# Optimization experiments

Hardware: AMD Instinct MI355X
Metric: run time of the kernel (lower is better)

The kernel has to match this reference:

```python
import jax, jax.numpy as jnp
import numpy as np

N, E, G = 50000, 400000, 64
F_IN, HID, HEADS, GF, NCLS = 16, 128, 4, 10, 6


def _init(k, shape, fan):
    return jax.random.normal(k, shape, jnp.float32) * (1.0 / np.sqrt(fan))


def setup_inputs() -> dict:
    key = jax.random.key(0)
    ks = jax.random.split(key, 16)
    x = jax.random.normal(ks[0], (N, F_IN), jnp.float32)
    edge_index = jax.random.randint(ks[1], (2, E), 0, N)
    batch = jnp.sort(jax.random.randint(ks[2], (N,), 0, G))
    graph_feat = jax.random.normal(ks[3], (G, GF), jnp.float32)
    # GATConv 1: in=16 -> heads=4, out=128, concat
    W1 = _init(ks[4], (F_IN, HEADS * HID), F_IN)
    att_src1 = _init(ks[5], (HEADS, HID), HID)
    att_dst1 = _init(ks[6], (HEADS, HID), HID)
    b1 = jnp.zeros((HEADS * HID,), jnp.float32)
    # GATConv 2: in=512 -> heads=1, out=128, mean (concat=False)
    W2 = _init(ks[7], (HEADS * HID, HID), HEADS * HID)
    att_src2 = _init(ks[8], (1, HID), HID)
    att_dst2 = _init(ks[9], (1, HID), HID)
    b2 = jnp.zeros((HID,), jnp.float32)
    # graph_proj MLP 10->32->32
    Wg1 = _init(ks[10], (GF, 32), GF); bg1 = jnp.zeros((32,), jnp.float32)
    Wg2 = _init(ks[11], (32, 32), 32); bg2 = jnp.zeros((32,), jnp.float32)
    # classifier 160->128->6
    Wc1 = _init(ks[12], (HID + 32, 128), HID + 32); bc1 = jnp.zeros((128,), jnp.float32)
    Wc2 = _init(ks[13], (128, NCLS), 128); bc2 = jnp.zeros((NCLS,), jnp.float32)
    return dict(x=x, edge_index=edge_index, batch=batch, graph_feat=graph_feat,
                W1=W1, att_src1=att_src1, att_dst1=att_dst1, b1=b1,
                W2=W2, att_src2=att_src2, att_dst2=att_dst2, b2=b2,
                Wg1=Wg1, bg1=bg1, Wg2=Wg2, bg2=bg2,
                Wc1=Wc1, bc1=bc1, Wc2=Wc2, bc2=bc2)


def gat_layer(x, W, att_src, att_dst, bias, src, dst, n_nodes, heads, out_dim, concat):
    # Linear transform: [N, H, C]
    h = (x @ W).reshape(n_nodes, heads, out_dim)
    a_src = jnp.einsum('nhc,hc->nh', h, att_src)  # [N,H]
    a_dst = jnp.einsum('nhc,hc->nh', h, att_dst)  # [N,H]
    e = jax.nn.leaky_relu(a_src[src] + a_dst[dst], 0.2)  # [Etot,H]
    # segment softmax over edges grouped by dst (self-loops ensure nonempty)
    m = jax.ops.segment_max(e, dst, num_segments=n_nodes)
    ex = jnp.exp(e - m[dst])
    denom = jax.ops.segment_sum(ex, dst, num_segments=n_nodes)
    alpha = ex / denom[dst]  # [Etot,H]
    out = jax.ops.segment_sum(alpha[:, :, None] * h[src], dst, num_segments=n_nodes)  # [N,H,C]
    if concat:
        out = out.reshape(n_nodes, heads * out_dim)
    else:
        out = out.mean(axis=1)
    return out + bias


def reference(x, edge_index, batch, graph_feat,
              W1, att_src1, att_dst1, b1,
              W2, att_src2, att_dst2, b2,
              Wg1, bg1, Wg2, bg2, Wc1, bc1, Wc2, bc2):
    n = x.shape[0]
    loops = jnp.arange(n, dtype=edge_index.dtype)
    src = jnp.concatenate([edge_index[0], loops])
    dst = jnp.concatenate([edge_index[1], loops])
    h = jax.nn.elu(gat_layer(x, W1, att_src1, att_dst1, b1, src, dst, n, HEADS, HID, True))
    h = jax.nn.elu(gat_layer(h, W2, att_src2, att_dst2, b2, src, dst, n, 1, HID, False))
    # global mean pool over graphs
    g = graph_feat.shape[0]
    sums = jax.ops.segment_sum(h, batch, num_segments=g)
    counts = jax.ops.segment_sum(jnp.ones((n, 1), h.dtype), batch, num_segments=g)
    pooled = sums / jnp.maximum(counts, 1.0)
    gf = jax.nn.relu(graph_feat @ Wg1 + bg1) @ Wg2 + bg2
    z = jnp.concatenate([pooled, gf], axis=1)
    z = jax.nn.relu(z @ Wc1 + bc1)
    return z @ Wc2 + bc2
```

## Files before the change

### kernel.cpp

```cpp
#include <hip/hip_runtime.h>
#include <hip/hip_bf16.h>

#define NN 50000
#define EE 400000
#define GG 64
#define CAP 48
#define HROW 520

typedef unsigned short u16;
typedef unsigned char u8;
typedef long long i64;
typedef unsigned long long u64;
typedef __attribute__((ext_vector_type(8))) short bf16x8;
typedef __attribute__((ext_vector_type(4))) float f32x4;
typedef __attribute__((ext_vector_type(2))) float f32x2;

__device__ __forceinline__ float b2f(u16 u) {
    unsigned int x = ((unsigned int)u) << 16;
    return __uint_as_float(x);
}
__device__ __forceinline__ u16 f2b(float f) {
    unsigned int x = __float_as_uint(f);
    unsigned int r = x + 0x7fffu + ((x >> 16) & 1u);
    return (u16)(r >> 16);
}
__device__ __forceinline__ u8 f2fp8(float f) {
    return (u8)(__builtin_amdgcn_cvt_pk_fp8_f32(f, f, 0, false) & 0xFF);
}
__device__ __forceinline__ f32x2 fp8x2_f32(unsigned int v, bool hi) {
    return hi ? __builtin_amdgcn_cvt_pk_f32_fp8(v, true)
              : __builtin_amdgcn_cvt_pk_f32_fp8(v, false);
}
__device__ __forceinline__ float wred_sum(float v) {
    #pragma unroll
    for (int o = 32; o; o >>= 1) v += __shfl_xor(v, o, 64);
    return v;
}
__device__ __forceinline__ float lrelu(float v) { return v > 0.f ? v : 0.2f * v; }

__global__ void k_prep(const int* __restrict__ batch, int* __restrict__ deg,
                       int* __restrict__ col, int* __restrict__ gstart,
                       const float* __restrict__ W1, const float* __restrict__ as1,
                       const float* __restrict__ ad1, u16* __restrict__ W1p,
                       const float* __restrict__ W2, u8* __restrict__ W2p,
                       float* __restrict__ pooled) {
    __shared__ float asw[16][8];
    int b = blockIdx.x, t = threadIdx.x;
    if (b < 196) {
        int n = b * 256 + t;
        if (n < NN) { deg[n] = 1; col[(size_t)n * CAP] = n; }
    } else if (b == 196) {
        if (t <= GG) {
            int lo = 0, hi = NN;
            while (lo < hi) {
                int mid = (lo + hi) >> 1;
                if (batch[mid] < t) lo = mid + 1; else hi = mid;
            }
            gstart[t] = lo;
        }
    } else if (b < 453) {
        int idx = (b - 197) * 256 + t;
        int j = idx & 7;
        int l = (idx >> 3) & 63;
        int ct = idx >> 9;
        int c = ct >> 3, tt = ct & 7;
        int p = c * 32 + (l >> 4) * 8 + j;
        int lp = p >> 3, jp = p & 7;
        int chan = 128 * (lp >> 4) + 16 * jp + (lp & 15);
        int n = tt * 16 + (l & 15);
        W2p[idx] = f2fp8(W2[chan * 128 + n]);
    } else if (b == 453) {
        int pair = t >> 1, half = t & 1;
        int k = pair >> 3, h = pair & 7;
        int hd = h & 3;
        const float* att = (h >= 4) ? ad1 : as1;
        float s = 0.f;
        int c0 = half * 64;
        for (int c = c0; c < c0 + 64; c++)
            s += W1[k * 512 + hd * 128 + c] * att[hd * 128 + c];
        s += __shfl_xor(s, 1, 64);
        if (half == 0) asw[k][h] = s;
        __syncthreads();
        for (int idx = t; idx < 33 * 64 * 8; idx += 256) {
            int j = idx & 7, l = (idx >> 3) & 63, tt = idx >> 9;
            int quad = l >> 4, m = l & 15;
            int k2 = quad * 8 + j;
            float v = 0.f;
            if (k2 < 16) {
                if (tt < 32) v = W1[k2 * 512 + tt * 16 + m];
                else if (m < 8) v = asw[k2][m];
            }
            W1p[idx] = f2b(v);
        }
    } else {
        for (int i = t; i < GG * 128; i += 256) pooled[i] = 0.f;
    }
}

__global__ void k_edges(const int* __restrict__ ei, int* __restrict__ deg,
                        int* __restrict__ col) {
    int e = blockIdx.x * 256 + threadIdx.x;
    if (e < EE) {
        int s = ei[e];
        int d = ei[EE + e];
        int slot = atomicAdd(&deg[d], 1);
        if (slot < CAP) col[(size_t)d * CAP + slot] = s;
    }
}

__global__ __launch_bounds__(256) void k_gemm1(
    const float* __restrict__ x, const u16* __restrict__ W1p,
    u8* __restrict__ h1, float* __restrict__ a_src1, float* __restrict__ a_dst1) {
    int tid = threadIdx.x;
    int wave = tid >> 6, l = tid & 63;
    int quad = l >> 4, m = l & 15;
    int row0 = blockIdx.x * 64 + wave * 16;
    int arow = row0 + m;
    int arow_c = arow < NN ? arow : (NN - 1);
    bf16x8 af;
    if (quad < 2) {
        const float* xp = x + arow_c * 16 + quad * 8;
        float4 x0 = *(const float4*)(xp);
        float4 x1 = *(const float4*)(xp + 4);
        u16 tmp[8] = {f2b(x0.x), f2b(x0.y), f2b(x0.z), f2b(x0.w),
                      f2b(x1.x), f2b(x1.y), f2b(x1.z), f2b(x1.w)};
        af = *(bf16x8*)tmp;
    } else {
        af = (bf16x8){0, 0, 0, 0, 0, 0, 0, 0};
    }
    const u16* bp = W1p + l * 8;
    f32x4 acc[33];
    #pragma unroll
    for (int tt = 0; tt < 33; tt++) acc[tt] = (f32x4){0.f, 0.f, 0.f, 0.f};
    #pragma unroll
    for (int tt = 0; tt < 33; tt++) {
        bf16x8 bf = *(const bf16x8*)(bp + (size_t)tt * 512);
        acc[tt] = __builtin_amdgcn_mfma_f32_16x16x32_bf16(af, bf, acc[tt], 0, 0, 0);
    }
    #pragma unroll
    for (int r = 0; r < 4; r++) {
        int row = row0 + quad * 4 + r;
        if (row >= NN) continue;
        unsigned int d[8];
        #pragma unroll
        for (int dd = 0; dd < 8; dd++) {
            unsigned int w = __builtin_amdgcn_cvt_pk_fp8_f32(acc[4 * dd][r], acc[4 * dd + 1][r], 0, false);
            w = __builtin_amdgcn_cvt_pk_fp8_f32(acc[4 * dd + 2][r], acc[4 * dd + 3][r], w, true);
            d[dd] = w;
        }
        uint4 v0; v0.x = d[0]; v0.y = d[1]; v0.z = d[2]; v0.w = d[3];
        uint4 v1; v1.x = d[4]; v1.y = d[5]; v1.z = d[6]; v1.w = d[7];
        *(uint4*)(h1 + (size_t)row * 512 + m * 32) = v0;
        *(uint4*)(h1 + (size_t)row * 512 + m * 32 + 16) = v1;
        float v = acc[32][r];
        if (m < 4) a_src1[row * 4 + m] = v;
        else if (m < 8) a_dst1[row * 4 + (m - 4)] = v;
    }
}

__global__ __launch_bounds__(256) void k_mid(
    const int* __restrict__ deg, const int* __restrict__ col,
    const float* __restrict__ a_src1, const float* __restrict__ a_dst1,
    const u8* __restrict__ h1, const float* __restrict__ b1,
    const u8* __restrict__ W2p, const float* __restrict__ as2,
    const float* __restrict__ ad2, u8* __restrict__ hL2,
    float* __restrict__ a_src2, float* __restrict__ a_dst2) {
    __shared__ u64 hrowq[16 * HROW / 8];
    __shared__ float alphaS[4][64][4];
    __shared__ float part[16][2][4];
    u8* hrow = (u8*)hrowq;
    int t = threadIdx.x;
    int w = t >> 6, l = t & 63;
    int n0 = blockIdx.x * 16;
    int g = l >> 4, m = l & 15;
    const u8* hb = h1 + m * 32 + g * 8;
    for (int i = 0; i < 4; i++) {
        int n = n0 + w * 4 + i;
        int dg = min(deg[n], CAP);
        int sl = (l < dg) ? col[(size_t)n * CAP + l] : 0;
        float4 ad = *(const float4*)(a_dst1 + n * 4);
        float4 as = *(const float4*)(a_src1 + (size_t)sl * 4);
        float4 e;
        e.x = __expf(lrelu(as.x + ad.x)); e.y = __expf(lrelu(as.y + ad.y));
        e.z = __expf(lrelu(as.z + ad.z)); e.w = __expf(lrelu(as.w + ad.w));
        if (l >= dg) e = (float4){0.f, 0.f, 0.f, 0.f};
        float4 inv;
        inv.x = 1.0f / wred_sum(e.x);
        inv.y = 1.0f / wred_sum(e.y);
        inv.z = 1.0f / wred_sum(e.z);
        inv.w = 1.0f / wred_sum(e.w);
        {
            float4 a4;
            a4.x = e.x * inv.x; a4.y = e.y * inv.y;
            a4.z = e.z * inv.z; a4.w = e.w * inv.w;
            *(float4*)&alphaS[w][l][0] = a4;
        }
        f32x2 acc[4] = {{0.f, 0.f}, {0.f, 0.f}, {0.f, 0.f}, {0.f, 0.f}};
        int iters = (dg + 3) >> 2;
        for (int j = 0; j < iters; j++) {
            int e0 = 4 * j, e1 = 4 * j + 1, e2 = 4 * j + 2, e3 = 4 * j + 3;
            int s0 = __shfl(sl, e0), s1 = __shfl(sl, e1);
            int s2 = __shfl(sl, e2), s3 = __shfl(sl, e3);
            float a0 = alphaS[w][e0][g], a1 = alphaS[w][e1][g];
            float a2 = alphaS[w][e2][g], a3 = alphaS[w][e3][g];
            uint2 u0 = *(const uint2*)(hb + (size_t)s0 * 512);
            uint2 u1 = *(const uint2*)(hb + (size_t)s1 * 512);
            uint2 u2 = *(const uint2*)(hb + (size_t)s2 * 512);
            uint2 u3 = *(const uint2*)(hb + (size_t)s3 * 512);
            acc[0] += a0 * fp8x2_f32(u0.x, false);
            acc[1] += a0 * fp8x2_f32(u0.x, true);
            acc[2] += a0 * fp8x2_f32(u0.y, false);
            acc[3] += a0 * fp8x2_f32(u0.y, true);
            acc[0] += a1 * fp8x2_f32(u1.x, false);
            acc[1] += a1 * fp8x2_f32(u1.x, true);
            acc[2] += a1 * fp8x2_f32(u1.y, false);
            acc[3] += a1 * fp8x2_f32(u1.y, true);
            acc[0] += a2 * fp8x2_f32(u2.x, false);
            acc[1] += a2 * fp8x2_f32(u2.x, true);
            acc[2] += a2 * fp8x2_f32(u2.y, false);
            acc[3] += a2 * fp8x2_f32(u2.y, true);
            acc[0] += a3 * fp8x2_f32(u3.x, false);
            acc[1] += a3 * fp8x2_f32(u3.x, true);
            acc[2] += a3 * fp8x2_f32(u3.y, false);
            acc[3] += a3 * fp8x2_f32(u3.y, true);
        }
        float av[8] = {acc[0].x, acc[0].y, acc[1].x, acc[1].y,
                       acc[2].x, acc[2].y, acc[3].x, acc[3].y};
        const float* bb = b1 + 128 * g + m;
        float v[8];
        #pragma unroll
        for (int j = 0; j < 8; j++) {
            float q = av[j] + bb[16 * j];
            v[j] = q > 0.f ? q : __expf(q) - 1.0f;
        }
        unsigned int d0 = __builtin_amdgcn_cvt_pk_fp8_f32(v[0], v[1], 0, false);
        d0 = __builtin_amdgcn_cvt_pk_fp8_f32(v[2], v[3], d0, true);
        unsigned int d1 = __builtin_amdgcn_cvt_pk_fp8_f32(v[4], v[5], 0, false);
        d1 = __builtin_amdgcn_cvt_pk_fp8_f32(v[6], v[7], d1, true);
        uint2 ov; ov.x = d0; ov.y = d1;
        *(uint2*)(hrow + (w * 4 + i) * HROW + l * 8) = ov;
    }
    __syncthreads();
    int quad = l >> 4;
    int tt0 = 2 * w;
    const u8* bbase = W2p + l * 8;
    f32x4 accA = (f32x4){0.f, 0.f, 0.f, 0.f};
    f32x4 accB = (f32x4){0.f, 0.f, 0.f, 0.f};
    #pragma unroll
    for (int c = 0; c < 16; c++) {
        i64 af = *(const i64*)(hrow + m * HROW + c * 32 + quad * 8);
        i64 bf0 = *(const i64*)(bbase + (size_t)(c * 8 + tt0) * 512);
        i64 bf1 = *(const i64*)(bbase + (size_t)(c * 8 + tt0 + 1) * 512);
        accA = __builtin_amdgcn_mfma_f32_16x16x32_fp8_fp8(af, bf0, accA, 0, 0, 0);
        accB = __builtin_amdgcn_mfma_f32_16x16x32_fp8_fp8(af, bf1, accB, 0, 0, 0);
    }
    float as0 = as2[tt0 * 16 + m], ad0 = ad2[tt0 * 16 + m];
    float as1v = as2[(tt0 + 1) * 16 + m], ad1v = ad2[(tt0 + 1) * 16 + m];
    #pragma unroll
    for (int r = 0; r < 4; r++) {
        int node = n0 + quad * 4 + r;
        float v0 = accA[r], v1 = accB[r];
        hL2[(size_t)node * 128 + tt0 * 16 + m] = f2fp8(v0);
        hL2[(size_t)node * 128 + (tt0 + 1) * 16 + m] = f2fp8(v1);
        float rs = v0 * as0 + v1 * as1v;
        float rd = v0 * ad0 + v1 * ad1v;
        #pragma unroll
        for (int o = 1; o < 16; o <<= 1) {
            rs += __shfl_xor(rs, o, 64);
            rd += __shfl_xor(rd, o, 64);
        }
        if (m == 0) { part[quad * 4 + r][0][w] = rs; part[quad * 4 + r][1][w] = rd; }
    }
    __syncthreads();
    if (t < 32) {
        int row = t >> 1, which = t & 1;
        float s = part[row][which][0] + part[row][which][1] +
                  part[row][which][2] + part[row][which][3];
        if (which) a_dst2[n0 + row] = s; else a_src2[n0 + row] = s;
    }
}

__global__ __launch_bounds__(256) void k_agg2(
    const int* __restrict__ deg, const int* __restrict__ col,
    const float* __restrict__ a_src2, const float* __restrict__ a_dst2,
    const u8* __restrict__ hL2, const float* __restrict__ b2v,
    const int* __restrict__ batch, float* __restrict__ pooled) {
    __shared__ float red[4][128];
    __shared__ int gS[4];
    int t = threadIdx.x;
    int wave = t >> 6, l = t & 63;
    int n = blockIdx.x * 4 + wave;
    if (n >= NN) return;
    int dg = min(deg[n], CAP);
    int sl = (l < dg) ? col[(size_t)n * CAP + l] : 0;
    float ad = a_dst2[n];
    float e = (l < dg) ? __expf(lrelu(a_src2[sl] + ad)) : 0.f;
    float inv = 1.0f / wred_sum(e);
    float al = e * inv;
    f32x2 acc = {0.f, 0.f};
    const u8* hb = hL2 + l * 2;
    int iters = (dg + 3) >> 2;
    for (int j = 0; j < iters; j++) {
        int e0 = 4 * j, e1 = 4 * j + 1, e2 = 4 * j + 2, e3 = 4 * j + 3;
        int s0 = __shfl(sl, e0), s1 = __shfl(sl, e1);
        int s2 = __shfl(sl, e2), s3 = __shfl(sl, e3);
        float a0 = __shfl(al, e0), a1 = __shfl(al, e1);
        float a2 = __shfl(al, e2), a3 = __shfl(al, e3);
        unsigned int u0 = *(const u16*)(hb + (size_t)s0 * 128);
        unsigned int u1 = *(const u16*)(hb + (size_t)s1 * 128);
        unsigned int u2 = *(const u16*)(hb + (size_t)s2 * 128);
        unsigned int u3 = *(const u16*)(hb + (size_t)s3 * 128);
        acc += a0 * fp8x2_f32(u0, false);
        acc += a1 * fp8x2_f32(u1, false);
        acc += a2 * fp8x2_f32(u2, false);
        acc += a3 * fp8x2_f32(u3, false);
    }
    float o0 = acc.x + b2v[2 * l];     o0 = o0 > 0.f ? o0 : __expf(o0) - 1.0f;
    float o1 = acc.y + b2v[2 * l + 1]; o1 = o1 > 0.f ? o1 : __expf(o1) - 1.0f;
    red[wave][2 * l] = o0;
    red[wave][2 * l + 1] = o1;
    if (l == 0) gS[wave] = batch[n];
    __syncthreads();
    if (t < 128) {
        int g0 = gS[0];
        if (gS[1] == g0 && gS[2] == g0 && gS[3] == g0) {
            float s = red[0][t] + red[1][t] + red[2][t] + red[3][t];
            atomicAdd(&pooled[g0 * 128 + t], s);
        } else {
            #pragma unroll
            for (int w = 0; w < 4; w++)
                atomicAdd(&pooled[gS[w] * 128 + t], red[w][t]);
        }
    }
}

__global__ __launch_bounds__(128) void k_head(
    const int* __restrict__ gstart, const float* __restrict__ pooled,
    const float* __restrict__ gfeat,
    const float* __restrict__ Wg1, const float* __restrict__ bg1,
    const float* __restrict__ Wg2, const float* __restrict__ bg2,
    const float* __restrict__ Wc1, const float* __restrict__ bc1,
    const float* __restrict__ Wc2, const float* __restrict__ bc2,
    float* __restrict__ out) {
    __shared__ float z[160];
    __shared__ float hg[32];
    __shared__ float c1b[128];
    int g = blockIdx.x, t = threadIdx.x;
    float cntf = (float)(gstart[g + 1] - gstart[g]);
    z[t] = pooled[g * 128 + t] / fmaxf(cntf, 1.0f);
    if (t < 32) {
        float a = bg1[t];
        for (int i = 0; i < 10; i++) a += gfeat[g * 10 + i] * Wg1[i * 32 + t];
        hg[t] = fmaxf(a, 0.f);
    }
    __syncthreads();
    if (t < 32) {
        float a = bg2[t];
        for (int i = 0; i < 32; i++) a += hg[i] * Wg2[i * 32 + t];
        z[128 + t] = a;
    }
    __syncthreads();
    float a = bc1[t];
    for (int i = 0; i < 160; i++) a += z[i] * Wc1[i * 128 + t];
    c1b[t] = fmaxf(a, 0.f);
    __syncthreads();
    if (t < 6) {
        float o = bc2[t];
        for (int i = 0; i < 128; i++) o += c1b[i] * Wc2[i * 6 + t];
        out[g * 6 + t] = o;
    }
}

extern "C" void kernel_launch(void* const* d_in, const int* in_sizes, int n_in,
                              void* d_out, int out_size, void* d_ws, size_t ws_size,
                              hipStream_t stream) {
    const float* x     = (const float*)d_in[0];
    const int*   ei    = (const int*)d_in[1];
    const int*   batch = (const int*)d_in[2];
    const float* gfeat = (const float*)d_in[3];
    const float* W1    = (const float*)d_in[4];
    const float* as1   = (const float*)d_in[5];
    const float* ad1   = (const float*)d_in[6];
    const float* b1    = (const float*)d_in[7];
    const float* W2    = (const float*)d_in[8];
    const float* as2   = (const float*)d_in[9];
    const float* ad2   = (const float*)d_in[10];
    const float* b2    = (const float*)d_in[11];
    const float* Wg1   = (const float*)d_in[12];
    const float* bg1   = (const float*)d_in[13];
    const float* Wg2   = (const float*)d_in[14];
    const float* bg2   = (const float*)d_in[15];
    const float* Wc1   = (const float*)d_in[16];
    const float* bc1   = (const float*)d_in[17];
    const float* Wc2   = (const float*)d_in[18];
    const float* bc2   = (const float*)d_in[19];
    float* out = (float*)d_out;

    size_t off = 0;
    char* base = (char*)d_ws;
    auto take = [&](size_t nbytes) -> char* {
        char* p = base + off;
        off = (off + nbytes + 255) & ~(size_t)255;
        return p;
    };
    u8*    h1     = (u8*)take((size_t)NN * 512);
    u8*    hL2    = (u8*)take((size_t)NN * 128);
    float* a_src1 = (float*)take((size_t)NN * 4 * 4);
    float* a_dst1 = (float*)take((size_t)NN * 4 * 4);
    float* a_src2 = (float*)take((size_t)NN * 4);
    float* a_dst2 = (float*)take((size_t)NN * 4);
    int*   deg    = (int*)take((size_t)NN * 4);
    int*   col    = (int*)take((size_t)NN * CAP * 4);
    float* pooled = (float*)take(GG * 128 * 4);
    int*   gstart = (int*)take((GG + 1) * 4);
    u8*    W2p    = (u8*)take((size_t)512 * 128);
    u16*   W1p    = (u16*)take((size_t)33 * 64 * 8 * 2);
    (void)ws_size; (void)in_sizes; (void)n_in; (void)out_size;

    k_prep<<<455, 256, 0, stream>>>(batch, deg, col, gstart, W1, as1, ad1, W1p,
                                    W2, W2p, pooled);
    k_edges<<<(EE + 255) / 256, 256, 0, stream>>>(ei, deg, col);
    k_gemm1<<<(NN + 63) / 64, 256, 0, stream>>>(x, W1p, h1, a_src1, a_dst1);
    k_mid<<<NN / 16, 256, 0, stream>>>(deg, col, a_src1, a_dst1, h1, b1,
                                       W2p, as2, ad2, hL2, a_src2, a_dst2);
    k_agg2<<<(NN + 3) / 4, 256, 0, stream>>>(deg, col, a_src2, a_dst2, hL2, b2,
                                             batch, pooled);
    k_head<<<GG, 128, 0, stream>>>(gstart, pooled, gfeat, Wg1, bg1, Wg2, bg2,
                                   Wc1, bc1, Wc2, bc2, out);
}
```

Measured before the change: 243.9 us.

## Assign one wave per node in k_mid with 1024-thread blocks

```diff
diff --git a/kernel.cpp b/kernel.cpp
--- a/kernel.cpp
+++ b/kernel.cpp
@@ -158,7 +158,7 @@
     }
 }
 
-__global__ __launch_bounds__(256) void k_mid(
+__global__ __launch_bounds__(1024) void k_mid(
     const int* __restrict__ deg, const int* __restrict__ col,
     const float* __restrict__ a_src1, const float* __restrict__ a_dst1,
     const u8* __restrict__ h1, const float* __restrict__ b1,
@@ -166,16 +166,15 @@
     const float* __restrict__ ad2, u8* __restrict__ hL2,
     float* __restrict__ a_src2, float* __restrict__ a_dst2) {
     __shared__ u64 hrowq[16 * HROW / 8];
-    __shared__ float alphaS[4][64][4];
-    __shared__ float part[16][2][4];
+    __shared__ float alphaS[16][64][4];
+    __shared__ float part[16][2][8];
     u8* hrow = (u8*)hrowq;
     int t = threadIdx.x;
     int w = t >> 6, l = t & 63;
     int n0 = blockIdx.x * 16;
     int g = l >> 4, m = l & 15;
-    const u8* hb = h1 + m * 32 + g * 8;
-    for (int i = 0; i < 4; i++) {
-        int n = n0 + w * 4 + i;
+    {
+        int n = n0 + w;
         int dg = min(deg[n], CAP);
         int sl = (l < dg) ? col[(size_t)n * CAP + l] : 0;
         float4 ad = *(const float4*)(a_dst1 + n * 4);
@@ -195,34 +194,28 @@
             a4.z = e.z * inv.z; a4.w = e.w * inv.w;
             *(float4*)&alphaS[w][l][0] = a4;
         }
+        const u8* hb = h1 + m * 32 + g * 8;
         f32x2 acc[4] = {{0.f, 0.f}, {0.f, 0.f}, {0.f, 0.f}, {0.f, 0.f}};
-        int iters = (dg + 3) >> 2;
+        int iters = (dg + 7) >> 3;
         for (int j = 0; j < iters; j++) {
-            int e0 = 4 * j, e1 = 4 * j + 1, e2 = 4 * j + 2, e3 = 4 * j + 3;
-            int s0 = __shfl(sl, e0), s1 = __shfl(sl, e1);
-            int s2 = __shfl(sl, e2), s3 = __shfl(sl, e3);
-            float a0 = alphaS[w][e0][g], a1 = alphaS[w][e1][g];
-            float a2 = alphaS[w][e2][g], a3 = alphaS[w][e3][g];
-            uint2 u0 = *(const uint2*)(hb + (size_t)s0 * 512);
-            uint2 u1 = *(const uint2*)(hb + (size_t)s1 * 512);
-            uint2 u2 = *(const uint2*)(hb + (size_t)s2 * 512);
-            uint2 u3 = *(const uint2*)(hb + (size_t)s3 * 512);
-            acc[0] += a0 * fp8x2_f32(u0.x, false);
-            acc[1] += a0 * fp8x2_f32(u0.x, true);
-            acc[2] += a0 * fp8x2_f32(u0.y, false);
-            acc[3] += a0 * fp8x2_f32(u0.y, true);
-            acc[0] += a1 * fp8x2_f32(u1.x, false);
-            acc[1] += a1 * fp8x2_f32(u1.x, true);
-            acc[2] += a1 * fp8x2_f32(u1.y, false);
-            acc[3] += a1 * fp8x2_f32(u1.y, true);
-            acc[0] += a2 * fp8x2_f32(u2.x, false);
-            acc[1] += a2 * fp8x2_f32(u2.x, true);
-            acc[2] += a2 * fp8x2_f32(u2.y, false);
-            acc[3] += a2 * fp8x2_f32(u2.y, true);
-            acc[0] += a3 * fp8x2_f32(u3.x, false);
-            acc[1] += a3 * fp8x2_f32(u3.x, true);
-            acc[2] += a3 * fp8x2_f32(u3.y, false);
-            acc[3] += a3 * fp8x2_f32(u3.y, true);
+            #pragma unroll
+            for (int q = 0; q < 8; q += 2) {
+                int eA = 8 * j + q, eB = 8 * j + q + 1;
+                int sA = __shfl(sl, eA);
+                int sB = __shfl(sl, eB);
+                float aA = alphaS[w][eA][g];
+                float aB = alphaS[w][eB][g];
+                uint2 uA = *(const uint2*)(hb + (size_t)sA * 512);
+                uint2 uB = *(const uint2*)(hb + (size_t)sB * 512);
+                acc[0] += aA * fp8x2_f32(uA.x, false);
+                acc[1] += aA * fp8x2_f32(uA.x, true);
+                acc[2] += aA * fp8x2_f32(uA.y, false);
+                acc[3] += aA * fp8x2_f32(uA.y, true);
+                acc[0] += aB * fp8x2_f32(uB.x, false);
+                acc[1] += aB * fp8x2_f32(uB.x, true);
+                acc[2] += aB * fp8x2_f32(uB.y, false);
+                acc[3] += aB * fp8x2_f32(uB.y, true);
+            }
         }
         float av[8] = {acc[0].x, acc[0].y, acc[1].x, acc[1].y,
                        acc[2].x, acc[2].y, acc[3].x, acc[3].y};
@@ -238,44 +231,42 @@
         unsigned int d1 = __builtin_amdgcn_cvt_pk_fp8_f32(v[4], v[5], 0, false);
         d1 = __builtin_amdgcn_cvt_pk_fp8_f32(v[6], v[7], d1, true);
         uint2 ov; ov.x = d0; ov.y = d1;
-        *(uint2*)(hrow + (w * 4 + i) * HROW + l * 8) = ov;
-    }
-    __syncthreads();
-    int quad = l >> 4;
-    int tt0 = 2 * w;
-    const u8* bbase = W2p + l * 8;
-    f32x4 accA = (f32x4){0.f, 0.f, 0.f, 0.f};
-    f32x4 accB = (f32x4){0.f, 0.f, 0.f, 0.f};
-    #pragma unroll
-    for (int c = 0; c < 16; c++) {
-        i64 af = *(const i64*)(hrow + m * HROW + c * 32 + quad * 8);
-        i64 bf0 = *(const i64*)(bbase + (size_t)(c * 8 + tt0) * 512);
-        i64 bf1 = *(const i64*)(bbase + (size_t)(c * 8 + tt0 + 1) * 512);
-        accA = __builtin_amdgcn_mfma_f32_16x16x32_fp8_fp8(af, bf0, accA, 0, 0, 0);
-        accB = __builtin_amdgcn_mfma_f32_16x16x32_fp8_fp8(af, bf1, accB, 0, 0, 0);
-    }
-    float as0 = as2[tt0 * 16 + m], ad0 = ad2[tt0 * 16 + m];
-    float as1v = as2[(tt0 + 1) * 16 + m], ad1v = ad2[(tt0 + 1) * 16 + m];
-    #pragma unroll
-    for (int r = 0; r < 4; r++) {
-        int node = n0 + quad * 4 + r;
-        float v0 = accA[r], v1 = accB[r];
-        hL2[(size_t)node * 128 + tt0 * 16 + m] = f2fp8(v0);
-        hL2[(size_t)node * 128 + (tt0 + 1) * 16 + m] = f2fp8(v1);
-        float rs = v0 * as0 + v1 * as1v;
-        float rd = v0 * ad0 + v1 * ad1v;
+        *(uint2*)(hrow + w * HROW + l * 8) = ov;
+    }
+    __syncthreads();
+    if (w < 8) {
+        int quad = l >> 4;
+        int tt = w;
+        const u8* bbase = W2p + l * 8;
+        f32x4 acc2 = (f32x4){0.f, 0.f, 0.f, 0.f};
         #pragma unroll
-        for (int o = 1; o < 16; o <<= 1) {
-            rs += __shfl_xor(rs, o, 64);
-            rd += __shfl_xor(rd, o, 64);
-        }
-        if (m == 0) { part[quad * 4 + r][0][w] = rs; part[quad * 4 + r][1][w] = rd; }
+        for (int c = 0; c < 16; c++) {
+            i64 af = *(const i64*)(hrow + m * HROW + c * 32 + quad * 8);
+            i64 bf = *(const i64*)(bbase + (size_t)(c * 8 + tt) * 512);
+            acc2 = __builtin_amdgcn_mfma_f32_16x16x32_fp8_fp8(af, bf, acc2, 0, 0, 0);
+        }
+        float asv = as2[tt * 16 + m], adv = ad2[tt * 16 + m];
+        #pragma unroll
+        for (int r = 0; r < 4; r++) {
+            int node = n0 + quad * 4 + r;
+            float v = acc2[r];
+            hL2[(size_t)node * 128 + tt * 16 + m] = f2fp8(v);
+            float rs = v * asv;
+            float rd = v * adv;
+            #pragma unroll
+            for (int o = 1; o < 16; o <<= 1) {
+                rs += __shfl_xor(rs, o, 64);
+                rd += __shfl_xor(rd, o, 64);
+            }
+            if (m == 0) { part[quad * 4 + r][0][w] = rs; part[quad * 4 + r][1][w] = rd; }
+        }
     }
     __syncthreads();
     if (t < 32) {
         int row = t >> 1, which = t & 1;
-        float s = part[row][which][0] + part[row][which][1] +
-                  part[row][which][2] + part[row][which][3];
+        float s = 0.f;
+        #pragma unroll
+        for (int i = 0; i < 8; i++) s += part[row][which][i];
         if (which) a_dst2[n0 + row] = s; else a_src2[n0 + row] = s;
     }
 }
@@ -421,8 +412,8 @@
                                     W2, W2p, pooled);
     k_edges<<<(EE + 255) / 256, 256, 0, stream>>>(ei, deg, col);
     k_gemm1<<<(NN + 63) / 64, 256, 0, stream>>>(x, W1p, h1, a_src1, a_dst1);
-    k_mid<<<NN / 16, 256, 0, stream>>>(deg, col, a_src1, a_dst1, h1, b1,
-                                       W2p, as2, ad2, hL2, a_src2, a_dst2);
+    k_mid<<<NN / 16, 1024, 0, stream>>>(deg, col, a_src1, a_dst1, h1, b1,
+                                        W2p, as2, ad2, hL2, a_src2, a_dst2);
     k_agg2<<<(NN + 3) / 4, 256, 0, stream>>>(deg, col, a_src2, a_dst2, hL2, b2,
                                              batch, pooled);
     k_head<<<GG, 128, 0, stream>>>(gstart, pooled, gfeat, Wg1, bg1, Wg2, bg2,
```

New measurement: 277.0 us. 1.14x slower.
